# Performance work log

Hardware: AMD Instinct MI355X
Metric: run time of the kernel (lower is better)

## Reference

```python
import jax, jax.numpy as jnp
import numpy as np

B, H, S, D = 4, 16, 2048, 64


def setup_inputs() -> dict:
    key = jax.random.key(0)
    kq, kk, kv = jax.random.split(key, 3)
    q = jax.random.normal(kq, (B, H, S, D), dtype=jnp.float32)
    k = jax.random.normal(kk, (B, H, S, D), dtype=jnp.float32)
    v = jax.random.normal(kv, (B, H, S, D), dtype=jnp.float32)
    mask = jnp.tril(jnp.ones((S, S), dtype=jnp.bool_))  # causal: True = attend
    return {"q": q, "k": k, "v": v, "mask": mask}


def reference(q, k, v, mask):
    d_k = q.shape[-1]
    scale = 1.0 / jnp.sqrt(jnp.asarray(d_k, q.dtype))
    # scores: [B, H, S_q, S_k] -- full O(N^2) matrix, faithful to original
    score = jnp.einsum('bhqd,bhkd->bhqk', q, k) * scale
    score = jnp.where(mask, score, jnp.asarray(-jnp.inf, score.dtype))
    attn = jax.nn.softmax(score, axis=-1)
    return jnp.einsum('bhqk,bhkd->bhqd', attn, v)
```

## Files before the change

kernel.cpp:

```cpp
#include <hip/hip_runtime.h>
#include <hip/hip_bf16.h>

typedef __attribute__((ext_vector_type(8))) short short8_t;
typedef __attribute__((ext_vector_type(16))) float f32x16;
typedef __attribute__((ext_vector_type(4))) unsigned uint4_t;

constexpr int S  = 2048;
constexpr int D  = 64;
constexpr int BQ = 128;
constexpr int KV = 64;
constexpr int NQ = S / BQ;
constexpr int NT = S / KV;
constexpr int BH_C = 64;
constexpr float THR = 8.f;

static __device__ __forceinline__ unsigned packbf(float lo, float hi) {
  __hip_bfloat162 p = __float22bfloat162_rn(float2{lo, hi});
  return (unsigned)__bfloat16_as_ushort(p.x) | ((unsigned)__bfloat16_as_ushort(p.y) << 16);
}
static __device__ __forceinline__ short8_t pack8(float4 a, float4 b) {
  uint4_t u = { packbf(a.x, a.y), packbf(a.z, a.w), packbf(b.x, b.y), packbf(b.z, b.w) };
  return __builtin_bit_cast(short8_t, u);
}
static __device__ __forceinline__ float vmax16(const f32x16& a) {
  float x0 = fmaxf(a[0], a[1]),   x1 = fmaxf(a[2], a[3]);
  float x2 = fmaxf(a[4], a[5]),   x3 = fmaxf(a[6], a[7]);
  float x4 = fmaxf(a[8], a[9]),   x5 = fmaxf(a[10], a[11]);
  float x6 = fmaxf(a[12], a[13]), x7 = fmaxf(a[14], a[15]);
  x0 = fmaxf(x0, x1); x2 = fmaxf(x2, x3); x4 = fmaxf(x4, x5); x6 = fmaxf(x6, x7);
  return fmaxf(fmaxf(x0, x2), fmaxf(x4, x6));
}

static __device__ __forceinline__ void plswap(unsigned &a, unsigned &b) {
  asm volatile("v_permlane32_swap_b32 %0, %1" : "+v"(a), "+v"(b));
}

static __device__ __forceinline__ void build_pfrags_pl(const f32x16& p,
                                                       short8_t& f0, short8_t& f1) {
  unsigned W0 = packbf(p[0],  p[1]),  W1 = packbf(p[2],  p[3]);
  unsigned W2 = packbf(p[4],  p[5]),  W3 = packbf(p[6],  p[7]);
  unsigned W4 = packbf(p[8],  p[9]),  W5 = packbf(p[10], p[11]);
  unsigned W6 = packbf(p[12], p[13]), W7 = packbf(p[14], p[15]);
  plswap(W0, W2); plswap(W1, W3);
  plswap(W4, W6); plswap(W5, W7);
  uint4_t u0 = { W0, W1, W2, W3 };
  uint4_t u1 = { W4, W5, W6, W7 };
  f0 = __builtin_bit_cast(short8_t, u0);
  f1 = __builtin_bit_cast(short8_t, u1);
}

static __device__ __forceinline__ void build_pfrags(const f32x16& p, int h,
                                                    short8_t& f0, short8_t& f1) {
  unsigned W0 = packbf(p[0],  p[1]),  W1 = packbf(p[2],  p[3]);
  unsigned W2 = packbf(p[4],  p[5]),  W3 = packbf(p[6],  p[7]);
  unsigned W4 = packbf(p[8],  p[9]),  W5 = packbf(p[10], p[11]);
  unsigned W6 = packbf(p[12], p[13]), W7 = packbf(p[14], p[15]);
  unsigned e0 = __shfl_xor(W0, 32), e1 = __shfl_xor(W1, 32);
  unsigned e2 = __shfl_xor(W2, 32), e3 = __shfl_xor(W3, 32);
  unsigned e4 = __shfl_xor(W4, 32), e5 = __shfl_xor(W5, 32);
  unsigned e6 = __shfl_xor(W6, 32), e7 = __shfl_xor(W7, 32);
  uint4_t u0, u1;
  if (h) { u0 = uint4_t{e2, e3, W2, W3}; u1 = uint4_t{e6, e7, W6, W7}; }
  else   { u0 = uint4_t{W0, W1, e0, e1}; u1 = uint4_t{W4, W5, e4, e5}; }
  f0 = __builtin_bit_cast(short8_t, u0);
  f1 = __builtin_bit_cast(short8_t, u1);
}

__global__ __launch_bounds__(256)
void prep_kernel(const float* __restrict__ k, const float* __restrict__ v,
                 short* __restrict__ kb, short* __restrict__ vtb)
{
  const int tile = (int)blockIdx.x;
  const int bh   = (int)blockIdx.y;
  const int tid  = (int)threadIdx.x;
  const int kv0  = tile * KV;
  const int srow = tid >> 2, sch = tid & 3;

  __shared__ float vt[KV][D + 4];

  {
    const float* kp = k + ((size_t)bh * S + kv0 + srow) * D + sch * 16;
    float4 a0 = *(const float4*)(kp);     float4 a1 = *(const float4*)(kp + 4);
    float4 a2 = *(const float4*)(kp + 8); float4 a3 = *(const float4*)(kp + 12);
    short* kd = kb + ((size_t)bh * S + kv0 + srow) * D;
    *(short8_t*)&kd[((2 * sch)     ^ (srow & 7)) * 8] = pack8(a0, a1);
    *(short8_t*)&kd[((2 * sch + 1) ^ (srow & 7)) * 8] = pack8(a2, a3);

    const float* vp = v + ((size_t)bh * S + kv0 + srow) * D + sch * 16;
    float4 b0 = *(const float4*)(vp);     float4 b1 = *(const float4*)(vp + 4);
    float4 b2 = *(const float4*)(vp + 8); float4 b3 = *(const float4*)(vp + 12);
    *(float4*)&vt[srow][sch * 16 + 0]  = b0;
    *(float4*)&vt[srow][sch * 16 + 4]  = b1;
    *(float4*)&vt[srow][sch * 16 + 8]  = b2;
    *(float4*)&vt[srow][sch * 16 + 12] = b3;
  }
  __syncthreads();
  {
    const int d = tid >> 2, q4 = tid & 3;
    float f[16];
    #pragma unroll
    for (int jj = 0; jj < 16; ++jj) f[jj] = vt[16 * q4 + jj][d];
    float4 c0 = make_float4(f[0],  f[1],  f[2],  f[3]);
    float4 c1 = make_float4(f[4],  f[5],  f[6],  f[7]);
    float4 c2 = make_float4(f[8],  f[9],  f[10], f[11]);
    float4 c3 = make_float4(f[12], f[13], f[14], f[15]);
    short* vd = vtb + (size_t)bh * S * D + (size_t)tile * KV * D + d * 64;
    *(short8_t*)&vd[((2 * q4)     ^ (d & 7)) * 8] = pack8(c0, c1);
    *(short8_t*)&vd[((2 * q4 + 1) ^ (d & 7)) * 8] = pack8(c2, c3);
  }
}

__global__ __launch_bounds__(256, 2)
void fattn17_kernel(const float* __restrict__ q, const short* __restrict__ kb,
                    const short* __restrict__ vtb, float* __restrict__ out)
{
  const int bid = (int)blockIdx.x;
  const int r4 = bid >> 8;
  const int g  = (bid >> 6) & 3;
  int qblk;
  if      (r4 == 0) qblk = 15 - g;
  else if (r4 == 1) qblk = g;
  else if (r4 == 2) qblk = 11 - g;
  else              qblk = 4 + g;
  const int bh   = bid & (BH_C - 1);
  const int tid  = (int)threadIdx.x;
  const int lane = tid & 63;
  const int wave = tid >> 6;
  const int h    = lane >> 5;
  const int ln   = lane & 31;

  const int qw = qblk * BQ + wave * 32;
  const int qi = qw + ln;
  const int qmax_w = qw + 31;
  const int ntseg = 2 * (qblk + 1);

  __shared__ short bufK[2][KV * D];
  __shared__ short bufV[2][KV * D];

  const short* kbase = kb  + (size_t)bh * S * D;
  const short* vbase = vtb + (size_t)bh * S * D;

  short8_t rk0, rk1, rv0, rv1;
  auto issue = [&](int t) {
    const short* gk = kbase + (size_t)t * (KV * D) + tid * 16;
    rk0 = *(const short8_t*)gk; rk1 = *(const short8_t*)(gk + 8);
    const short* gv = vbase + (size_t)t * (KV * D) + tid * 16;
    rv0 = *(const short8_t*)gv; rv1 = *(const short8_t*)(gv + 8);
  };
  issue(0);
  int cur = 0;

  const float qscale = 0.125f * 1.4426950408889634f;

  short8_t aq[4];
  {
    const float* qp = q + ((size_t)bh * S + qi) * D + 8 * h;
    #pragma unroll
    for (int ks = 0; ks < 4; ++ks) {
      float4 lo = *(const float4*)(qp + 16 * ks);
      float4 hi = *(const float4*)(qp + 16 * ks + 4);
      lo.x *= qscale; lo.y *= qscale; lo.z *= qscale; lo.w *= qscale;
      hi.x *= qscale; hi.y *= qscale; hi.z *= qscale; hi.w *= qscale;
      aq[ks] = pack8(lo, hi);
    }
  }

  f32x16 o0, o1;
  #pragma unroll
  for (int r = 0; r < 16; ++r) { o0[r] = 0.f; o1[r] = 0.f; }
  float lsum = 0.f;

  #pragma unroll 1
  for (int i = 0; i < ntseg; ++i) {
    {
      short* dK = &bufK[cur][tid * 16];
      *(short8_t*)dK = rk0; *(short8_t*)(dK + 8) = rk1;
      short* dV = &bufV[cur][tid * 16];
      *(short8_t*)dV = rv0; *(short8_t*)(dV + 8) = rv1;
    }
    if (i + 1 < ntseg) issue(i + 1);
    asm volatile("s_waitcnt lgkmcnt(0)" ::: "memory");
    __builtin_amdgcn_s_barrier();
    __builtin_amdgcn_sched_barrier(0);

    const int kv0 = i * KV;
    if (kv0 <= qmax_w) {
      const bool hi_live = (kv0 + 32 <= qmax_w);
      const short* Kc = bufK[cur];
      const short* Vc = bufV[cur];

      f32x16 st0, st1;
      #pragma unroll
      for (int r = 0; r < 16; ++r) { st0[r] = 0.f; st1[r] = 0.f; }
      __builtin_amdgcn_s_setprio(1);
      #pragma unroll
      for (int ks = 0; ks < 4; ++ks) {
        short8_t kf0 = *(const short8_t*)&Kc[ln * D + (((2 * ks + h) ^ (ln & 7)) * 8)];
        st0 = __builtin_amdgcn_mfma_f32_32x32x16_bf16(kf0, aq[ks], st0, 0, 0, 0);
      }
      if (hi_live) {
        #pragma unroll
        for (int ks = 0; ks < 4; ++ks) {
          short8_t kf1 = *(const short8_t*)&Kc[(32 + ln) * D + (((2 * ks + h) ^ (ln & 7)) * 8)];
          st1 = __builtin_amdgcn_mfma_f32_32x32x16_bf16(kf1, aq[ks], st1, 0, 0, 0);
        }
      }
      __builtin_amdgcn_s_setprio(0);

      if (kv0 + KV - 1 > qw) {
        #pragma unroll
        for (int r = 0; r < 16; ++r) {
          const int kvr = kv0 + (r & 3) + 8 * (r >> 2) + 4 * h;
          st0[r] = (kvr > qi) ? -INFINITY : st0[r];
          if (hi_live) st1[r] = (kvr + 32 > qi) ? -INFINITY : st1[r];
        }
      }

      float s0 = 0.f, s1 = 0.f, s2 = 0.f, s3 = 0.f;
      #pragma unroll
      for (int r = 0; r < 16; r += 4) {
        st0[r]     = exp2f(st0[r]);     s0 += st0[r];
        st0[r + 1] = exp2f(st0[r + 1]); s1 += st0[r + 1];
        st0[r + 2] = exp2f(st0[r + 2]); s2 += st0[r + 2];
        st0[r + 3] = exp2f(st0[r + 3]); s3 += st0[r + 3];
      }
      if (hi_live) {
        #pragma unroll
        for (int r = 0; r < 16; r += 4) {
          st1[r]     = exp2f(st1[r]);     s0 += st1[r];
          st1[r + 1] = exp2f(st1[r + 1]); s1 += st1[r + 1];
          st1[r + 2] = exp2f(st1[r + 2]); s2 += st1[r + 2];
          st1[r + 3] = exp2f(st1[r + 3]); s3 += st1[r + 3];
        }
      }
      lsum += (s0 + s1) + (s2 + s3);

      short8_t p00, p01, p10, p11;
      build_pfrags_pl(st0, p00, p01);
      if (hi_live) build_pfrags_pl(st1, p10, p11);
      __builtin_amdgcn_s_setprio(1);
      #pragma unroll
      for (int dt = 0; dt < 2; ++dt) {
        const int dr = 32 * dt + ln;
        f32x16 &o = dt ? o1 : o0;
        short8_t vf00 = *(const short8_t*)&Vc[dr * 64 + (((0 + h) ^ (dr & 7)) * 8)];
        short8_t vf01 = *(const short8_t*)&Vc[dr * 64 + (((2 + h) ^ (dr & 7)) * 8)];
        o = __builtin_amdgcn_mfma_f32_32x32x16_bf16(vf00, p00, o, 0, 0, 0);
        o = __builtin_amdgcn_mfma_f32_32x32x16_bf16(vf01, p01, o, 0, 0, 0);
        if (hi_live) {
          short8_t vf10 = *(const short8_t*)&Vc[dr * 64 + (((4 + h) ^ (dr & 7)) * 8)];
          short8_t vf11 = *(const short8_t*)&Vc[dr * 64 + (((6 + h) ^ (dr & 7)) * 8)];
          o = __builtin_amdgcn_mfma_f32_32x32x16_bf16(vf10, p10, o, 0, 0, 0);
          o = __builtin_amdgcn_mfma_f32_32x32x16_bf16(vf11, p11, o, 0, 0, 0);
        }
      }
      __builtin_amdgcn_s_setprio(0);
    }
    cur ^= 1;
  }

  lsum += __shfl_xor(lsum, 32);
  const float inv = 1.f / fmaxf(lsum, 1e-37f);
  float* op = out + ((size_t)bh * S + qi) * D;
  #pragma unroll
  for (int r = 0; r < 16; ++r) {
    const int dr = (r & 3) + 8 * (r >> 2) + 4 * h;
    op[dr]      = o0[r] * inv;
    op[32 + dr] = o1[r] * inv;
  }
}

__global__ __launch_bounds__(256, 2)
void fattn3_kernel(const float* __restrict__ q, const float* __restrict__ k,
                   const float* __restrict__ v, float* __restrict__ out)
{
  const int pair = (int)blockIdx.x;
  const int bh   = (int)blockIdx.y;
  const int tid  = (int)threadIdx.x;
  const int wave = tid >> 6;
  const int lane = tid & 63;
  const int h    = lane >> 5;
  const int ln   = lane & 31;

  __shared__ short smem[BQ * D];
  short* Ks = smem;
  short* Vs = smem + KV * D;

  const float qscale = 0.125f * 1.4426950408889634f;
  const int srow = tid >> 2;
  const int sch  = tid & 3;

  #pragma unroll 1
  for (int seg = 0; seg < 2; ++seg) {
    const int qblk = seg ? (NQ - 1 - pair) : pair;
    const int qb = qblk * BQ;
    const int qw = qb + wave * 32;
    const int qi = qw + ln;
    const int qmax_w = qw + 31;
    const int kv_end = qb + BQ;

    __syncthreads();
    {
      const int r  = tid >> 1;
      const int h2 = tid & 1;
      const float* qp = q + ((size_t)bh * S + qb + r) * D + h2 * 32;
      #pragma unroll
      for (int jq = 0; jq < 4; ++jq) {
        float4 a = *(const float4*)(qp + jq * 8);
        float4 b = *(const float4*)(qp + jq * 8 + 4);
        a.x *= qscale; a.y *= qscale; a.z *= qscale; a.w *= qscale;
        b.x *= qscale; b.y *= qscale; b.z *= qscale; b.w *= qscale;
        *(short8_t*)&smem[r * D + (((4 * h2 + jq) ^ (r & 7)) * 8)] = pack8(a, b);
      }
    }
    __syncthreads();

    short8_t aq[4];
    {
      const int R = wave * 32 + ln;
      #pragma unroll
      for (int ks = 0; ks < 4; ++ks)
        aq[ks] = *(const short8_t*)&smem[R * D + (((2 * ks + h) ^ (R & 7)) * 8)];
    }
    __syncthreads();

    f32x16 o0, o1;
    #pragma unroll
    for (int r = 0; r < 16; ++r) { o0[r] = 0.f; o1[r] = 0.f; }
    float m = -INFINITY, lsum = 0.f;

    for (int kv0 = 0; kv0 < kv_end; kv0 += KV) {
      const float* kp = k + ((size_t)bh * S + kv0 + srow) * D + sch * 16;
      const float* vp = v + ((size_t)bh * S + kv0 + srow) * D + sch * 16;
      float4 k0 = *(const float4*)(kp);     float4 k1 = *(const float4*)(kp + 4);
      float4 k2 = *(const float4*)(kp + 8); float4 k3 = *(const float4*)(kp + 12);
      float4 v0 = *(const float4*)(vp);     float4 v1 = *(const float4*)(vp + 4);
      float4 v2 = *(const float4*)(vp + 8); float4 v3 = *(const float4*)(vp + 12);

      __syncthreads();
      *(short8_t*)&Ks[srow * D + (((2 * sch)     ^ (srow & 7)) * 8)] = pack8(k0, k1);
      *(short8_t*)&Ks[srow * D + (((2 * sch + 1) ^ (srow & 7)) * 8)] = pack8(k2, k3);
      {
        float vf[16] = { v0.x,v0.y,v0.z,v0.w, v1.x,v1.y,v1.z,v1.w,
                         v2.x,v2.y,v2.z,v2.w, v3.x,v3.y,v3.z,v3.w };
        #pragma unroll
        for (int jv = 0; jv < 16; jv += 2) {
          const unsigned pw = packbf(vf[jv], vf[jv + 1]);
          const int d0 = 16 * sch + jv, d1 = d0 + 1;
          Vs[d0 * 64 + (((srow >> 3) ^ (d0 & 7)) * 8) + (srow & 7)] = (short)(pw & 0xffffu);
          Vs[d1 * 64 + (((srow >> 3) ^ (d1 & 7)) * 8) + (srow & 7)] = (short)(pw >> 16);
        }
      }
      __syncthreads();

      if (kv0 <= qmax_w) {
        const bool hi_live = (kv0 + 32 <= qmax_w);
        f32x16 st0, st1;
        #pragma unroll
        for (int r = 0; r < 16; ++r) { st0[r] = 0.f; st1[r] = 0.f; }
        #pragma unroll
        for (int ks = 0; ks < 4; ++ks) {
          short8_t kf0 = *(const short8_t*)&Ks[ln * D + (((2 * ks + h) ^ (ln & 7)) * 8)];
          st0 = __builtin_amdgcn_mfma_f32_32x32x16_bf16(kf0, aq[ks], st0, 0, 0, 0);
        }
        if (hi_live) {
          #pragma unroll
          for (int ks = 0; ks < 4; ++ks) {
            short8_t kf1 = *(const short8_t*)&Ks[(32 + ln) * D + (((2 * ks + h) ^ (ln & 7)) * 8)];
            st1 = __builtin_amdgcn_mfma_f32_32x32x16_bf16(kf1, aq[ks], st1, 0, 0, 0);
          }
        }
        if (kv0 + KV - 1 > qw) {
          #pragma unroll
          for (int r = 0; r < 16; ++r) {
            const int kvr = kv0 + (r & 3) + 8 * (r >> 2) + 4 * h;
            st0[r] = (kvr > qi) ? -INFINITY : st0[r];
            if (hi_live) st1[r] = (kvr + 32 > qi) ? -INFINITY : st1[r];
          }
        }
        float tm = hi_live ? fmaxf(vmax16(st0), vmax16(st1)) : vmax16(st0);
        tm = fmaxf(tm, __shfl_xor(tm, 32));
        if (!__all(tm <= m + THR)) {
          const float mn = fmaxf(m, tm);
          const float al = exp2f(m - mn);
          m = mn;
          lsum *= al;
          #pragma unroll
          for (int r = 0; r < 16; ++r) { o0[r] *= al; o1[r] *= al; }
        }
        float ssum = 0.f;
        #pragma unroll
        for (int r = 0; r < 16; ++r) { st0[r] = exp2f(st0[r] - m); ssum += st0[r]; }
        if (hi_live) {
          #pragma unroll
          for (int r = 0; r < 16; ++r) { st1[r] = exp2f(st1[r] - m); ssum += st1[r]; }
        }
        ssum += __shfl_xor(ssum, 32);
        lsum += ssum;

        short8_t p00, p01, p10, p11;
        build_pfrags(st0, h, p00, p01);
        if (hi_live) build_pfrags(st1, h, p10, p11);
        #pragma unroll
        for (int dt = 0; dt < 2; ++dt) {
          const int dr = 32 * dt + ln;
          f32x16 &o = dt ? o1 : o0;
          short8_t vf00 = *(const short8_t*)&Vs[dr * 64 + (((0 + h) ^ (dr & 7)) * 8)];
          short8_t vf01 = *(const short8_t*)&Vs[dr * 64 + (((2 + h) ^ (dr & 7)) * 8)];
          o = __builtin_amdgcn_mfma_f32_32x32x16_bf16(vf00, p00, o, 0, 0, 0);
          o = __builtin_amdgcn_mfma_f32_32x32x16_bf16(vf01, p01, o, 0, 0, 0);
          if (hi_live) {
            short8_t vf10 = *(const short8_t*)&Vs[dr * 64 + (((4 + h) ^ (dr & 7)) * 8)];
            short8_t vf11 = *(const short8_t*)&Vs[dr * 64 + (((6 + h) ^ (dr & 7)) * 8)];
            o = __builtin_amdgcn_mfma_f32_32x32x16_bf16(vf10, p10, o, 0, 0, 0);
            o = __builtin_amdgcn_mfma_f32_32x32x16_bf16(vf11, p11, o, 0, 0, 0);
          }
        }
      }
    }

    const float inv = 1.f / fmaxf(lsum, 1e-37f);
    float* op = out + ((size_t)bh * S + qi) * D;
    #pragma unroll
    for (int r = 0; r < 16; ++r) {
      const int dr = (r & 3) + 8 * (r >> 2) + 4 * h;
      op[dr]      = o0[r] * inv;
      op[32 + dr] = o1[r] * inv;
    }
  }
}

extern "C" void kernel_launch(void* const* d_in, const int* in_sizes, int n_in,
                              void* d_out, int out_size, void* d_ws, size_t ws_size,
                              hipStream_t stream) {
  const float* q = (const float*)d_in[0];
  const float* k = (const float*)d_in[1];
  const float* v = (const float*)d_in[2];
  float* out = (float*)d_out;
  const int BH = in_sizes[0] / (S * D);
  const size_t need = (size_t)BH * S * D * 2 * 2;
  if (BH == BH_C && ws_size >= need) {
    short* kbw  = (short*)d_ws;
    short* vtbw = kbw + (size_t)BH * S * D;
    prep_kernel<<<dim3(NT, BH), 256, 0, stream>>>(k, v, kbw, vtbw);
    fattn17_kernel<<<dim3(NQ * BH), 256, 0, stream>>>(q, kbw, vtbw, out);
  } else {
    fattn3_kernel<<<dim3(NQ / 2, BH), 256, 0, stream>>>(q, k, v, out);
  }
}
```

Baseline: 85.34 us.

## Software-pipeline QK^T of next tile with softmax/PV of current tile

Restructures the main loop into a two-stage software pipeline. The QK^T MFMAs for tile t+1 are issued before the exp/softmax and PV work of tile t, with two score register sets ping-ponged and the loop unrolled by two. This is meant to let the matrix units overlap with the exp and packing ALU work. In exchange it adds an extra barrier per tile and more live registers (four f32x16 score accumulators), which may pressure occupancy at the two-blocks-per-CU launch bound.

```diff
diff --git a/kernel.cpp b/kernel.cpp
--- a/kernel.cpp
+++ b/kernel.cpp
@@ -34,7 +34,6 @@
 static __device__ __forceinline__ void plswap(unsigned &a, unsigned &b) {
   asm volatile("v_permlane32_swap_b32 %0, %1" : "+v"(a), "+v"(b));
 }
-
 static __device__ __forceinline__ void build_pfrags_pl(const f32x16& p,
                                                        short8_t& f0, short8_t& f1) {
   unsigned W0 = packbf(p[0],  p[1]),  W1 = packbf(p[2],  p[3]);
@@ -48,7 +47,6 @@
   f0 = __builtin_bit_cast(short8_t, u0);
   f1 = __builtin_bit_cast(short8_t, u1);
 }
-
 static __device__ __forceinline__ void build_pfrags(const f32x16& p, int h,
                                                     short8_t& f0, short8_t& f1) {
   unsigned W0 = packbf(p[0],  p[1]),  W1 = packbf(p[2],  p[3]);
@@ -111,7 +109,7 @@
 }
 
 __global__ __launch_bounds__(256, 2)
-void fattn17_kernel(const float* __restrict__ q, const short* __restrict__ kb,
+void fattn18_kernel(const float* __restrict__ q, const short* __restrict__ kb,
                     const short* __restrict__ vtb, float* __restrict__ out)
 {
   const int bid = (int)blockIdx.x;
@@ -147,8 +145,12 @@
     const short* gv = vbase + (size_t)t * (KV * D) + tid * 16;
     rv0 = *(const short8_t*)gv; rv1 = *(const short8_t*)(gv + 8);
   };
-  issue(0);
-  int cur = 0;
+  auto stage = [&](short* dKb, short* dVb) {
+    short* dK = dKb + tid * 16;
+    *(short8_t*)dK = rk0; *(short8_t*)(dK + 8) = rk1;
+    short* dV = dVb + tid * 16;
+    *(short8_t*)dV = rv0; *(short8_t*)(dV + 8) = rv1;
+  };
 
   const float qscale = 0.125f * 1.4426950408889634f;
 
@@ -170,93 +172,115 @@
   for (int r = 0; r < 16; ++r) { o0[r] = 0.f; o1[r] = 0.f; }
   float lsum = 0.f;
 
-  #pragma unroll 1
-  for (int i = 0; i < ntseg; ++i) {
-    {
-      short* dK = &bufK[cur][tid * 16];
-      *(short8_t*)dK = rk0; *(short8_t*)(dK + 8) = rk1;
-      short* dV = &bufV[cur][tid * 16];
-      *(short8_t*)dV = rv0; *(short8_t*)(dV + 8) = rv1;
-    }
-    if (i + 1 < ntseg) issue(i + 1);
+  auto produce = [&](const short* Kc, f32x16& st0, f32x16& st1, bool hi) {
+    #pragma unroll
+    for (int r = 0; r < 16; ++r) { st0[r] = 0.f; st1[r] = 0.f; }
+    __builtin_amdgcn_s_setprio(1);
+    #pragma unroll
+    for (int ks = 0; ks < 4; ++ks) {
+      short8_t kf0 = *(const short8_t*)&Kc[ln * D + (((2 * ks + h) ^ (ln & 7)) * 8)];
+      st0 = __builtin_amdgcn_mfma_f32_32x32x16_bf16(kf0, aq[ks], st0, 0, 0, 0);
+    }
+    if (hi) {
+      #pragma unroll
+      for (int ks = 0; ks < 4; ++ks) {
+        short8_t kf1 = *(const short8_t*)&Kc[(32 + ln) * D + (((2 * ks + h) ^ (ln & 7)) * 8)];
+        st1 = __builtin_amdgcn_mfma_f32_32x32x16_bf16(kf1, aq[ks], st1, 0, 0, 0);
+      }
+    }
+    __builtin_amdgcn_s_setprio(0);
+  };
+
+  auto consume = [&](f32x16& st0, f32x16& st1, const short* Vc, int t) {
+    const int kv0 = t * KV;
+    const bool hi_live = (kv0 + 32 <= qmax_w);
+    if (kv0 + KV - 1 > qw) {
+      #pragma unroll
+      for (int r = 0; r < 16; ++r) {
+        const int kvr = kv0 + (r & 3) + 8 * (r >> 2) + 4 * h;
+        st0[r] = (kvr > qi) ? -INFINITY : st0[r];
+        if (hi_live) st1[r] = (kvr + 32 > qi) ? -INFINITY : st1[r];
+      }
+    }
+    float s0 = 0.f, s1 = 0.f, s2 = 0.f, s3 = 0.f;
+    #pragma unroll
+    for (int r = 0; r < 16; r += 4) {
+      st0[r]     = exp2f(st0[r]);     s0 += st0[r];
+      st0[r + 1] = exp2f(st0[r + 1]); s1 += st0[r + 1];
+      st0[r + 2] = exp2f(st0[r + 2]); s2 += st0[r + 2];
+      st0[r + 3] = exp2f(st0[r + 3]); s3 += st0[r + 3];
+    }
+    if (hi_live) {
+      #pragma unroll
+      for (int r = 0; r < 16; r += 4) {
+        st1[r]     = exp2f(st1[r]);     s0 += st1[r];
+        st1[r + 1] = exp2f(st1[r + 1]); s1 += st1[r + 1];
+        st1[r + 2] = exp2f(st1[r + 2]); s2 += st1[r + 2];
+        st1[r + 3] = exp2f(st1[r + 3]); s3 += st1[r + 3];
+      }
+    }
+    lsum += (s0 + s1) + (s2 + s3);
+
+    short8_t p00, p01, p10, p11;
+    build_pfrags_pl(st0, p00, p01);
+    if (hi_live) build_pfrags_pl(st1, p10, p11);
+    __builtin_amdgcn_s_setprio(1);
+    #pragma unroll
+    for (int dt = 0; dt < 2; ++dt) {
+      const int dr = 32 * dt + ln;
+      f32x16 &o = dt ? o1 : o0;
+      short8_t vf00 = *(const short8_t*)&Vc[dr * 64 + (((0 + h) ^ (dr & 7)) * 8)];
+      short8_t vf01 = *(const short8_t*)&Vc[dr * 64 + (((2 + h) ^ (dr & 7)) * 8)];
+      o = __builtin_amdgcn_mfma_f32_32x32x16_bf16(vf00, p00, o, 0, 0, 0);
+      o = __builtin_amdgcn_mfma_f32_32x32x16_bf16(vf01, p01, o, 0, 0, 0);
+      if (hi_live) {
+        short8_t vf10 = *(const short8_t*)&Vc[dr * 64 + (((4 + h) ^ (dr & 7)) * 8)];
+        short8_t vf11 = *(const short8_t*)&Vc[dr * 64 + (((6 + h) ^ (dr & 7)) * 8)];
+        o = __builtin_amdgcn_mfma_f32_32x32x16_bf16(vf10, p10, o, 0, 0, 0);
+        o = __builtin_amdgcn_mfma_f32_32x32x16_bf16(vf11, p11, o, 0, 0, 0);
+      }
+    }
+    __builtin_amdgcn_s_setprio(0);
+  };
+
+  auto lgkm_barrier = [&]() {
     asm volatile("s_waitcnt lgkmcnt(0)" ::: "memory");
     __builtin_amdgcn_s_barrier();
     __builtin_amdgcn_sched_barrier(0);
-
-    const int kv0 = i * KV;
-    if (kv0 <= qmax_w) {
-      const bool hi_live = (kv0 + 32 <= qmax_w);
-      const short* Kc = bufK[cur];
-      const short* Vc = bufV[cur];
-
-      f32x16 st0, st1;
-      #pragma unroll
-      for (int r = 0; r < 16; ++r) { st0[r] = 0.f; st1[r] = 0.f; }
-      __builtin_amdgcn_s_setprio(1);
-      #pragma unroll
-      for (int ks = 0; ks < 4; ++ks) {
-        short8_t kf0 = *(const short8_t*)&Kc[ln * D + (((2 * ks + h) ^ (ln & 7)) * 8)];
-        st0 = __builtin_amdgcn_mfma_f32_32x32x16_bf16(kf0, aq[ks], st0, 0, 0, 0);
-      }
-      if (hi_live) {
-        #pragma unroll
-        for (int ks = 0; ks < 4; ++ks) {
-          short8_t kf1 = *(const short8_t*)&Kc[(32 + ln) * D + (((2 * ks + h) ^ (ln & 7)) * 8)];
-          st1 = __builtin_amdgcn_mfma_f32_32x32x16_bf16(kf1, aq[ks], st1, 0, 0, 0);
-        }
-      }
-      __builtin_amdgcn_s_setprio(0);
-
-      if (kv0 + KV - 1 > qw) {
-        #pragma unroll
-        for (int r = 0; r < 16; ++r) {
-          const int kvr = kv0 + (r & 3) + 8 * (r >> 2) + 4 * h;
-          st0[r] = (kvr > qi) ? -INFINITY : st0[r];
-          if (hi_live) st1[r] = (kvr + 32 > qi) ? -INFINITY : st1[r];
-        }
-      }
-
-      float s0 = 0.f, s1 = 0.f, s2 = 0.f, s3 = 0.f;
-      #pragma unroll
-      for (int r = 0; r < 16; r += 4) {
-        st0[r]     = exp2f(st0[r]);     s0 += st0[r];
-        st0[r + 1] = exp2f(st0[r + 1]); s1 += st0[r + 1];
-        st0[r + 2] = exp2f(st0[r + 2]); s2 += st0[r + 2];
-        st0[r + 3] = exp2f(st0[r + 3]); s3 += st0[r + 3];
-      }
-      if (hi_live) {
-        #pragma unroll
-        for (int r = 0; r < 16; r += 4) {
-          st1[r]     = exp2f(st1[r]);     s0 += st1[r];
-          st1[r + 1] = exp2f(st1[r + 1]); s1 += st1[r + 1];
-          st1[r + 2] = exp2f(st1[r + 2]); s2 += st1[r + 2];
-          st1[r + 3] = exp2f(st1[r + 3]); s3 += st1[r + 3];
-        }
-      }
-      lsum += (s0 + s1) + (s2 + s3);
-
-      short8_t p00, p01, p10, p11;
-      build_pfrags_pl(st0, p00, p01);
-      if (hi_live) build_pfrags_pl(st1, p10, p11);
-      __builtin_amdgcn_s_setprio(1);
-      #pragma unroll
-      for (int dt = 0; dt < 2; ++dt) {
-        const int dr = 32 * dt + ln;
-        f32x16 &o = dt ? o1 : o0;
-        short8_t vf00 = *(const short8_t*)&Vc[dr * 64 + (((0 + h) ^ (dr & 7)) * 8)];
-        short8_t vf01 = *(const short8_t*)&Vc[dr * 64 + (((2 + h) ^ (dr & 7)) * 8)];
-        o = __builtin_amdgcn_mfma_f32_32x32x16_bf16(vf00, p00, o, 0, 0, 0);
-        o = __builtin_amdgcn_mfma_f32_32x32x16_bf16(vf01, p01, o, 0, 0, 0);
-        if (hi_live) {
-          short8_t vf10 = *(const short8_t*)&Vc[dr * 64 + (((4 + h) ^ (dr & 7)) * 8)];
-          short8_t vf11 = *(const short8_t*)&Vc[dr * 64 + (((6 + h) ^ (dr & 7)) * 8)];
-          o = __builtin_amdgcn_mfma_f32_32x32x16_bf16(vf10, p10, o, 0, 0, 0);
-          o = __builtin_amdgcn_mfma_f32_32x32x16_bf16(vf11, p11, o, 0, 0, 0);
-        }
-      }
-      __builtin_amdgcn_s_setprio(0);
-    }
-    cur ^= 1;
+  };
+
+  f32x16 stA0, stA1, stB0, stB1;
+  issue(0);
+  stage(bufK[0], bufV[0]);
+  if (1 < ntseg) issue(1);
+  lgkm_barrier();
+  produce(bufK[0], stA0, stA1, (32 <= qmax_w));
+
+  #pragma unroll 1
+  for (int ii = 0; ii < ntseg; ii += 2) {
+    lgkm_barrier();
+    if (ii + 1 < ntseg) {
+      stage(bufK[1], bufV[1]);
+      if (ii + 2 < ntseg) issue(ii + 2);
+    }
+    lgkm_barrier();
+    const int t1 = ii + 1;
+    if (t1 < ntseg && t1 * KV <= qmax_w)
+      produce(bufK[1], stB0, stB1, (t1 * KV + 32 <= qmax_w));
+    if (ii * KV <= qmax_w)
+      consume(stA0, stA1, bufV[0], ii);
+
+    lgkm_barrier();
+    if (ii + 2 < ntseg) {
+      stage(bufK[0], bufV[0]);
+      if (ii + 3 < ntseg) issue(ii + 3);
+    }
+    lgkm_barrier();
+    const int t2 = ii + 2;
+    if (t2 < ntseg && t2 * KV <= qmax_w)
+      produce(bufK[0], stA0, stA1, (t2 * KV + 32 <= qmax_w));
+    if (t1 < ntseg && t1 * KV <= qmax_w)
+      consume(stB0, stB1, bufV[1], t1);
   }
 
   lsum += __shfl_xor(lsum, 32);
@@ -443,7 +467,7 @@
     short* kbw  = (short*)d_ws;
     short* vtbw = kbw + (size_t)BH * S * D;
     prep_kernel<<<dim3(NT, BH), 256, 0, stream>>>(k, v, kbw, vtbw);
-    fattn17_kernel<<<dim3(NQ * BH), 256, 0, stream>>>(q, kbw, vtbw, out);
+    fattn18_kernel<<<dim3(NQ * BH), 256, 0, stream>>>(q, kbw, vtbw, out);
   } else {
     fattn3_kernel<<<dim3(NQ / 2, BH), 256, 0, stream>>>(q, k, v, out);
   }
```

Result: slower. 98.48 us (+15.4%).
